# Kernel optimization log

Hardware: AMD Instinct MI355X
Metric: run time of the kernel (lower is better)

Reference implementation:

```python
import jax, jax.numpy as jnp
import numpy as np

FEATURE_SIZE = 128
NUM_BINS = 5
HIDDEN = 512
CONTEXT = 64
N = 65536
PI = float(np.pi)
TAIL_BOUND = 5.0
MIN_BW = 1e-3
MIN_BH = 1e-3
MIN_D = 1e-3

_circ = np.array([1] * 64 + [0] * 64)
_trans = np.array(([0] * 32 + [1] * 32) * 2)
_fi = np.arange(FEATURE_SIZE)
IDX_IC = jnp.array(_fi[(_trans <= 0) & (_circ > 0)])   # identity circular (32)
IDX_IR = jnp.array(_fi[(_trans <= 0) & (_circ <= 0)])  # identity regular (32)
IDX_TC = jnp.array(_fi[(_trans > 0) & (_circ > 0)])    # transform circular (32)
IDX_TR = jnp.array(_fi[(_trans > 0) & (_circ <= 0)])   # transform regular (32)
NET_IN = 2 * IDX_IC.shape[0] + IDX_IR.shape[0]                                  # 96
NET_OUT = IDX_TC.shape[0] * NUM_BINS * 3 + IDX_TR.shape[0] * (NUM_BINS * 3 + 1) # 992


def _rq_spline(x, uw, uh, ud, left, right, bottom, top):
    """Monotonic rational-quadratic spline (nflows-style), forward direction.
    x: [N, D]; uw, uh: [N, D, K]; ud: [N, D, K+1]. Returns (y, logabsdet)."""
    K = uw.shape[-1]
    widths = jax.nn.softmax(uw, axis=-1)
    widths = MIN_BW + (1.0 - MIN_BW * K) * widths
    cumw = jnp.concatenate([jnp.zeros(widths.shape[:-1] + (1,), widths.dtype),
                            jnp.cumsum(widths, axis=-1)], axis=-1)
    cumw = left + (right - left) * cumw
    cumw = cumw.at[..., -1].set(right)
    widths = cumw[..., 1:] - cumw[..., :-1]

    heights = jax.nn.softmax(uh, axis=-1)
    heights = MIN_BH + (1.0 - MIN_BH * K) * heights
    cumh = jnp.concatenate([jnp.zeros(heights.shape[:-1] + (1,), heights.dtype),
                            jnp.cumsum(heights, axis=-1)], axis=-1)
    cumh = bottom + (top - bottom) * cumh
    cumh = cumh.at[..., -1].set(top)
    heights = cumh[..., 1:] - cumh[..., :-1]

    derivs = MIN_D + jax.nn.softplus(ud)  # [N, D, K+1]
    delta = heights / widths              # bin slopes

    xc = jnp.clip(x, left, right)
    # per-element bin search over knot positions
    idx = jnp.clip(jnp.sum(xc[..., None] >= cumw[..., 1:], axis=-1), 0, K - 1)

    def g(a, i):
        return jnp.take_along_axis(a, i[..., None], axis=-1)[..., 0]

    in_cw = g(cumw[..., :-1], idx)
    in_w = g(widths, idx)
    in_ch = g(cumh[..., :-1], idx)
    in_h = g(heights, idx)
    in_delta = g(delta, idx)
    d_k = g(derivs, idx)
    d_k1 = g(derivs, idx + 1)

    theta = (xc - in_cw) / in_w
    omt = 1.0 - theta
    num = in_h * (in_delta * theta * theta + d_k * theta * omt)
    den = in_delta + (d_k + d_k1 - 2.0 * in_delta) * theta * omt
    y = in_ch + num / den
    dnum = in_delta * in_delta * (d_k1 * theta * theta
                                  + 2.0 * in_delta * theta * omt
                                  + d_k * omt * omt)
    logabsdet = jnp.log(dnum) - 2.0 * jnp.log(den)
    return y, logabsdet


def setup_inputs() -> dict:
    key = jax.random.key(0)
    ks = jax.random.split(key, 6)
    inputs = jax.random.uniform(ks[0], (N, FEATURE_SIZE), jnp.float32)
    context = jax.random.normal(ks[1], (N, CONTEXT), jnp.float32)
    fan1 = NET_IN + CONTEXT
    W1 = jax.random.normal(ks[2], (fan1, HIDDEN), jnp.float32) / np.sqrt(fan1)
    b1 = jnp.zeros((HIDDEN,), jnp.float32)
    W2 = jax.random.normal(ks[3], (HIDDEN, HIDDEN), jnp.float32) / np.sqrt(HIDDEN)
    b2 = jnp.zeros((HIDDEN,), jnp.float32)
    W3 = jax.random.normal(ks[4], (HIDDEN, NET_OUT), jnp.float32) / np.sqrt(HIDDEN)
    b3 = jnp.zeros((NET_OUT,), jnp.float32)
    return {"inputs": inputs, "context": context,
            "W1": W1, "b1": b1, "W2": W2, "b2": b2, "W3": W3, "b3": b3}


def reference(inputs, context, W1, b1, W2, b2, W3, b3):
    ic = inputs[..., IDX_IC]
    ir = inputs[..., IDX_IR]
    tc = inputs[..., IDX_TC]
    tr = inputs[..., IDX_TR]

    # conditioner MLP on [cos(ic), sin(ic), ir, context]
    net_in = jnp.concatenate([jnp.cos(ic), jnp.sin(ic), ir, context], axis=-1)
    h = jax.nn.relu(net_in @ W1 + b1)
    h = jax.nn.relu(h @ W2 + b2)
    params = h @ W3 + b3  # [N, 992]

    ntc = IDX_TC.shape[0]
    ntr = IDX_TR.shape[0]
    K = NUM_BINS
    scale = 1.0 / np.sqrt(HIDDEN)

    cc = params[..., : ntc * 3 * K].reshape(-1, ntc, 3 * K)
    cr = params[..., ntc * 3 * K:].reshape(-1, ntr, 3 * K + 1)

    # circular spline on [-pi, pi] with periodic derivative (K derivs, wrap first)
    uw_c = cc[..., :K] * scale
    uh_c = cc[..., K:2 * K] * scale
    ud_c = cc[..., 2 * K:]
    ud_c = jnp.concatenate([ud_c, ud_c[..., :1]], axis=-1)
    yc, lad_c = _rq_spline(tc, uw_c, uh_c, ud_c, -PI, PI, -PI, PI)

    # regular spline on [-B, B] with K+1 derivatives; identity (linear tails) outside
    uw_r = cr[..., :K] * scale
    uh_r = cr[..., K:2 * K] * scale
    ud_r = cr[..., 2 * K:]
    inside = (tr >= -TAIL_BOUND) & (tr <= TAIL_BOUND)
    yr0, lad_r0 = _rq_spline(tr, uw_r, uh_r, ud_r,
                             -TAIL_BOUND, TAIL_BOUND, -TAIL_BOUND, TAIL_BOUND)
    yr = jnp.where(inside, yr0, tr)
    lad_r = jnp.where(inside, lad_r0, 0.0)

    outputs = jnp.zeros_like(inputs)
    outputs = outputs.at[..., IDX_IC].set(ic)
    outputs = outputs.at[..., IDX_IR].set(ir)
    outputs = outputs.at[..., IDX_TC].set(yc)
    outputs = outputs.at[..., IDX_TR].set(yr)
    logabsdet = jnp.sum(lad_c, axis=-1) + jnp.sum(lad_r, axis=-1)
    return outputs, logabsdet
```

## Files before the change

### kernel.cpp

```cpp
#include <hip/hip_runtime.h>
#include <hip/hip_bf16.h>
#include <cstdint>
#include <cstddef>


#define BM 128
#define BN 128
#define BK 64

typedef float  f32x4 __attribute__((ext_vector_type(4)));
typedef short  s16x8 __attribute__((ext_vector_type(8)));

__device__ __forceinline__ void mfma_bf16_16x16x32(f32x4& acc, s16x8 a, s16x8 b) {
    asm volatile("v_mfma_f32_16x16x32_bf16 %0, %1, %2, %0"
                 : "+v"(acc) : "v"(a), "v"(b));
}

__device__ __forceinline__ void gload_lds16(const void* g, void* lds) {
    __builtin_amdgcn_global_load_lds((const __attribute__((address_space(1))) void*)g,
                                     (__attribute__((address_space(3))) void*)lds,
                                     16, 0, 0);
}

__device__ __forceinline__ float bf2f(short s) {
    union { unsigned u; float f; } v;
    v.u = ((unsigned)(unsigned short)s) << 16;
    return v.f;
}


__global__ void prep_input_kernel(const float* __restrict__ inputs,
                                  const float* __restrict__ context,
                                  __hip_bfloat16* __restrict__ netin)
{
    const int n = blockIdx.x;
    const int c = threadIdx.x;
    float v;
    if (c < 32)       v = cosf(inputs[(size_t)n * 128 + c]);
    else if (c < 64)  v = sinf(inputs[(size_t)n * 128 + (c - 32)]);
    else if (c < 96)  v = inputs[(size_t)n * 128 + c];
    else if (c < 160) v = context[(size_t)n * 64 + (c - 96)];
    else              v = 0.f;
    netin[(size_t)n * 192 + c] = __float2bfloat16(v);
}

__global__ void prep_weights_kernel(const float* __restrict__ W1,
                                    const float* __restrict__ W2,
                                    const float* __restrict__ W3,
                                    const float* __restrict__ b3,
                                    __hip_bfloat16* __restrict__ W1T,
                                    __hip_bfloat16* __restrict__ W2T,
                                    __hip_bfloat16* __restrict__ W3T,
                                    float* __restrict__ b3p)
{
    const int T1 = 512 * 192, T2 = 512 * 512, T3 = 1024 * 512;
    const int total = T1 + T2 + T3 + 1024;
    for (int t = blockIdx.x * blockDim.x + threadIdx.x; t < total;
         t += gridDim.x * blockDim.x) {
        if (t < T1) {
            int nn = t / 192, k = t % 192;
            float v = (k < 160) ? W1[(size_t)k * 512 + nn] : 0.f;
            W1T[t] = __float2bfloat16(v);
        } else if (t < T1 + T2) {
            int u = t - T1;
            int nn = u / 512, k = u % 512;
            W2T[u] = __float2bfloat16(W2[(size_t)k * 512 + nn]);
        } else if (t < T1 + T2 + T3) {
            int u = t - T1 - T2;
            int nn = u / 512, k = u % 512;
            float v = (nn < 992) ? W3[(size_t)k * 992 + nn] : 0.f;
            W3T[u] = __float2bfloat16(v);
        } else {
            int u = t - T1 - T2 - T3;
            b3p[u] = (u < 992) ? b3[u] : 0.f;
        }
    }
}


template<bool RELU>
__global__ __launch_bounds__(256)
void gemm_bt_kernel(const __hip_bfloat16* __restrict__ A,
                    const __hip_bfloat16* __restrict__ BT,
                    const float* __restrict__ bias,
                    __hip_bfloat16* __restrict__ C,
                    int M, int Nc, int K)
{
    __shared__ __align__(16) short Ald[BM * BK];
    __shared__ __align__(16) short Bld[BN * BK];

    const int tid  = threadIdx.x;
    const int wid  = tid >> 6;
    const int lane = tid & 63;
    const int row0 = blockIdx.y * BM;
    const int col0 = blockIdx.x * BN;
    const int wr   = (wid >> 1) * 64;
    const int wc   = (wid & 1) * 64;

    f32x4 acc[4][4] = {};

    const int srow  = lane >> 3;
    const int scolb = (lane & 7) * 16;

    const char* Abase = (const char*)A  + (size_t)row0 * K * 2;
    const char* Bbase = (const char*)BT + (size_t)col0 * K * 2;

    const int fr = lane & 15;
    const int fq = lane >> 4;

    const int nk = K / BK;
    for (int kt = 0; kt < nk; ++kt) {
        __syncthreads();
#pragma unroll
        for (int i = 0; i < 4; ++i) {
            const int chunk = i * 4 + wid;
            const int r = chunk * 8 + srow;
            gload_lds16(Abase + ((size_t)r * K + (size_t)kt * BK) * 2 + scolb,
                        (char*)Ald + chunk * 1024);
            gload_lds16(Bbase + ((size_t)r * K + (size_t)kt * BK) * 2 + scolb,
                        (char*)Bld + chunk * 1024);
        }
        __syncthreads();
#pragma unroll
        for (int kk = 0; kk < 2; ++kk) {
            s16x8 af[4], bfv[4];
#pragma unroll
            for (int m = 0; m < 4; ++m)
                af[m] = *(const s16x8*)&Ald[(wr + m * 16 + fr) * BK + kk * 32 + fq * 8];
#pragma unroll
            for (int n = 0; n < 4; ++n)
                bfv[n] = *(const s16x8*)&Bld[(wc + n * 16 + fr) * BK + kk * 32 + fq * 8];
#pragma unroll
            for (int m = 0; m < 4; ++m)
#pragma unroll
                for (int n = 0; n < 4; ++n)
                    mfma_bf16_16x16x32(acc[m][n], af[m], bfv[n]);
        }
    }

#pragma unroll
    for (int n = 0; n < 4; ++n) {
        const int col = col0 + wc + n * 16 + fr;
        const float bv = bias[col];
#pragma unroll
        for (int m = 0; m < 4; ++m) {
            const int rbase = row0 + wr + m * 16 + fq * 4;
#pragma unroll
            for (int r = 0; r < 4; ++r) {
                float v = acc[m][n][r] + bv;
                if (RELU) v = fmaxf(v, 0.f);
                C[(size_t)(rbase + r) * Nc + col] = __float2bfloat16(v);
            }
        }
    }
}


__global__ __launch_bounds__(256)
void spline_kernel(const float* __restrict__ inputs,
                   const __hip_bfloat16* __restrict__ params,
                   float* __restrict__ out, int Nrows)
{
    __shared__ __align__(16) short plds[4][1024];
    const int wid  = threadIdx.x >> 6;
    const int lane = threadIdx.x & 63;
    const int row  = blockIdx.x * 4 + wid;

    const short* prow = (const short*)params + (size_t)row * 1024;
    for (int c = lane; c < 124; c += 64)
        ((int4*)&plds[wid][0])[c] = ((const int4*)prow)[c];
    __syncthreads();

    const bool circ = lane < 32;
    const int  j    = circ ? lane : lane - 32;
    const float PI_F  = 3.14159265358979323846f;
    const float left  = circ ? -PI_F : -5.0f;
    const float right = -left;
    const float SCALE = 0.04419417382415922f;

    const short* pp = &plds[wid][circ ? j * 15 : 480 + j * 16];

    float uw[5], uh[5], ud[6];
#pragma unroll
    for (int i = 0; i < 5; ++i) uw[i] = bf2f(pp[i]) * SCALE;
#pragma unroll
    for (int i = 0; i < 5; ++i) uh[i] = bf2f(pp[5 + i]) * SCALE;
    if (circ) {
#pragma unroll
        for (int i = 0; i < 5; ++i) ud[i] = bf2f(pp[10 + i]);
        ud[5] = ud[0];
    } else {
#pragma unroll
        for (int i = 0; i < 6; ++i) ud[i] = bf2f(pp[10 + i]);
    }

    const int xcol = circ ? (32 + j) : (96 + j);
    const float x  = inputs[(size_t)row * 128 + xcol];

    float mx = uw[0];
#pragma unroll
    for (int i = 1; i < 5; ++i) mx = fmaxf(mx, uw[i]);
    float e[5], s = 0.f;
#pragma unroll
    for (int i = 0; i < 5; ++i) { e[i] = __expf(uw[i] - mx); s += e[i]; }
    const float inv_s = 1.f / s;
    float cw[6];
    cw[0] = left;
    {
        float accw = 0.f;
#pragma unroll
        for (int i = 0; i < 5; ++i) {
            float wn = 0.001f + 0.995f * (e[i] * inv_s);
            accw += wn;
            cw[i + 1] = left + (right - left) * accw;
        }
    }
    cw[5] = right;

    float mh = uh[0];
#pragma unroll
    for (int i = 1; i < 5; ++i) mh = fmaxf(mh, uh[i]);
    float eh[5], sh = 0.f;
#pragma unroll
    for (int i = 0; i < 5; ++i) { eh[i] = __expf(uh[i] - mh); sh += eh[i]; }
    const float inv_sh = 1.f / sh;
    float ch[6];
    ch[0] = left;
    {
        float acch = 0.f;
#pragma unroll
        for (int i = 0; i < 5; ++i) {
            float hn = 0.001f + 0.995f * (eh[i] * inv_sh);
            acch += hn;
            ch[i + 1] = left + (right - left) * acch;
        }
    }
    ch[5] = right;

    float d[6];
#pragma unroll
    for (int i = 0; i < 6; ++i) {
        float u  = ud[i];
        float sp = fmaxf(u, 0.f) + log1pf(__expf(-fabsf(u)));
        d[i] = 0.001f + sp;
    }

    const float xc = fminf(fmaxf(x, left), right);
    int b = 0;
#pragma unroll
    for (int i = 1; i <= 5; ++i) b += (xc >= cw[i]) ? 1 : 0;
    b = (b > 4) ? 4 : b;

    float l_cw = cw[0], r_cw = cw[1], l_ch = ch[0], r_ch = ch[1], dk = d[0], dk1 = d[1];
#pragma unroll
    for (int i = 1; i < 5; ++i) {
        if (b == i) {
            l_cw = cw[i]; r_cw = cw[i + 1];
            l_ch = ch[i]; r_ch = ch[i + 1];
            dk   = d[i];  dk1  = d[i + 1];
        }
    }

    const float iw  = r_cw - l_cw;
    const float ih  = r_ch - l_ch;
    const float del = ih / iw;
    const float th  = (xc - l_cw) / iw;
    const float omt = 1.f - th;
    const float num = ih * (del * th * th + dk * th * omt);
    const float den = del + (dk + dk1 - 2.f * del) * th * omt;
    float y = l_ch + num / den;
    const float dnum = del * del * (dk1 * th * th + 2.f * del * th * omt + dk * omt * omt);
    float lad = __logf(dnum) - 2.f * __logf(den);

    if (!circ) {
        const bool inside = (x >= -5.0f) && (x <= 5.0f);
        if (!inside) { y = x; lad = 0.f; }
    }

    const int ccol = circ ? j : 64 + j;
    out[(size_t)row * 128 + ccol] = inputs[(size_t)row * 128 + ccol];
    out[(size_t)row * 128 + xcol] = y;

    float t = lad;
#pragma unroll
    for (int o = 32; o > 0; o >>= 1) t += __shfl_xor(t, o, 64);
    if (lane == 0) out[(size_t)Nrows * 128 + row] = t;
}


extern "C" void kernel_launch(void* const* d_in, const int* in_sizes, int n_in,
                              void* d_out, int out_size, void* d_ws, size_t ws_size,
                              hipStream_t stream)
{
    const float* inputs  = (const float*)d_in[0];
    const float* context = (const float*)d_in[1];
    const float* W1 = (const float*)d_in[2];
    const float* b1 = (const float*)d_in[3];
    const float* W2 = (const float*)d_in[4];
    const float* b2 = (const float*)d_in[5];
    const float* W3 = (const float*)d_in[6];
    const float* b3 = (const float*)d_in[7];
    float* out = (float*)d_out;

    const int Nrows = in_sizes[0] / 128;

    char* ws = (char*)d_ws;
    const size_t szh    = (size_t)Nrows * 512 * 2;
    const size_t sznet  = (size_t)Nrows * 192 * 2;
    const size_t szpar  = (size_t)Nrows * 1024 * 2;
    const size_t off_h2     = 0;
    const size_t off_netin  = szh;
    const size_t off_h1     = szh + sznet;
    const size_t off_params = szh;
    const size_t off_w1t    = szh + szpar;
    const size_t off_w2t    = off_w1t + (size_t)512 * 192 * 2;
    const size_t off_w3t    = off_w2t + (size_t)512 * 512 * 2;
    const size_t off_b3p    = off_w3t + (size_t)1024 * 512 * 2;

    __hip_bfloat16* netin  = (__hip_bfloat16*)(ws + off_netin);
    __hip_bfloat16* h1     = (__hip_bfloat16*)(ws + off_h1);
    __hip_bfloat16* h2     = (__hip_bfloat16*)(ws + off_h2);
    __hip_bfloat16* params = (__hip_bfloat16*)(ws + off_params);
    __hip_bfloat16* W1T    = (__hip_bfloat16*)(ws + off_w1t);
    __hip_bfloat16* W2T    = (__hip_bfloat16*)(ws + off_w2t);
    __hip_bfloat16* W3T    = (__hip_bfloat16*)(ws + off_w3t);
    float*          b3p    = (float*)(ws + off_b3p);

    prep_weights_kernel<<<2048, 256, 0, stream>>>(W1, W2, W3, b3, W1T, W2T, W3T, b3p);
    prep_input_kernel<<<Nrows, 192, 0, stream>>>(inputs, context, netin);

    gemm_bt_kernel<true ><<<dim3(4, Nrows / 128), 256, 0, stream>>>(
        netin, W1T, b1, h1, Nrows, 512, 192);
    gemm_bt_kernel<true ><<<dim3(4, Nrows / 128), 256, 0, stream>>>(
        h1, W2T, b2, h2, Nrows, 512, 512);
    gemm_bt_kernel<false><<<dim3(8, Nrows / 128), 256, 0, stream>>>(
        h2, W3T, b3p, params, Nrows, 1024, 512);

    spline_kernel<<<Nrows / 4, 256, 0, stream>>>(inputs, params, out, Nrows);
}
```

Before: 305.7 us.

## Fuse input prep, three-layer MLP and spline into one per-tile kernel

Replaces the separate prep, three GEMM and spline kernels with one kernel that processes 64 rows per block. Activations stay in swizzled LDS across layers and the final layer is split into two halves so each spline half reads parameters from LDS. W3 and the bias are repacked so each feature's parameters sit at a 16-element stride. This removes the global round trips for the hidden activations and parameters. In exchange it uses about 152KB of LDS per block, which allows only one block per CU with 8 waves, and the weights are read directly from global/L2 by every block without LDS staging.

```diff
diff --git a/kernel.cpp b/kernel.cpp
--- a/kernel.cpp
+++ b/kernel.cpp
@@ -4,45 +4,20 @@
 #include <cstddef>
 
 
-#define BM 128
-#define BN 128
-#define BK 64
-
 typedef float  f32x4 __attribute__((ext_vector_type(4)));
 typedef short  s16x8 __attribute__((ext_vector_type(8)));
 
-__device__ __forceinline__ void mfma_bf16_16x16x32(f32x4& acc, s16x8 a, s16x8 b) {
-    asm volatile("v_mfma_f32_16x16x32_bf16 %0, %1, %2, %0"
-                 : "+v"(acc) : "v"(a), "v"(b));
-}
-
-__device__ __forceinline__ void gload_lds16(const void* g, void* lds) {
-    __builtin_amdgcn_global_load_lds((const __attribute__((address_space(1))) void*)g,
-                                     (__attribute__((address_space(3))) void*)lds,
-                                     16, 0, 0);
-}
-
+__device__ __forceinline__ void mfma16(f32x4& acc, s16x8 a, s16x8 b) {
+    asm volatile("v_mfma_f32_16x16x32_bf16 %0, %1, %2, %0" : "+v"(acc) : "v"(a), "v"(b));
+}
 __device__ __forceinline__ float bf2f(short s) {
-    union { unsigned u; float f; } v;
-    v.u = ((unsigned)(unsigned short)s) << 16;
-    return v.f;
-}
-
-
-__global__ void prep_input_kernel(const float* __restrict__ inputs,
-                                  const float* __restrict__ context,
-                                  __hip_bfloat16* __restrict__ netin)
-{
-    const int n = blockIdx.x;
-    const int c = threadIdx.x;
-    float v;
-    if (c < 32)       v = cosf(inputs[(size_t)n * 128 + c]);
-    else if (c < 64)  v = sinf(inputs[(size_t)n * 128 + (c - 32)]);
-    else if (c < 96)  v = inputs[(size_t)n * 128 + c];
-    else if (c < 160) v = context[(size_t)n * 64 + (c - 96)];
-    else              v = 0.f;
-    netin[(size_t)n * 192 + c] = __float2bfloat16(v);
-}
+    union { unsigned u; float f; } v; v.u = ((unsigned)(unsigned short)s) << 16; return v.f;
+}
+__device__ __forceinline__ short f2bf(float f) {
+    __hip_bfloat16 h = __float2bfloat16(f); return *(short*)&h;
+}
+__device__ __forceinline__ int swz(int row) { return ((row ^ (row >> 3)) & 7) << 4; }
+
 
 __global__ void prep_weights_kernel(const float* __restrict__ W1,
                                     const float* __restrict__ W2,
@@ -67,135 +42,102 @@
             W2T[u] = __float2bfloat16(W2[(size_t)k * 512 + nn]);
         } else if (t < T1 + T2 + T3) {
             int u = t - T1 - T2;
-            int nn = u / 512, k = u % 512;
-            float v = (nn < 992) ? W3[(size_t)k * 992 + nn] : 0.f;
+            int c = u / 512, k = u % 512;
+            int f = c >> 4, p = c & 15;
+            float v = 0.f;
+            if (f < 32) { if (p < 15) v = W3[(size_t)k * 992 + f * 15 + p]; }
+            else        {              v = W3[(size_t)k * 992 + 480 + (f - 32) * 16 + p]; }
             W3T[u] = __float2bfloat16(v);
         } else {
-            int u = t - T1 - T2 - T3;
-            b3p[u] = (u < 992) ? b3[u] : 0.f;
-        }
-    }
-}
-
-
-template<bool RELU>
-__global__ __launch_bounds__(256)
-void gemm_bt_kernel(const __hip_bfloat16* __restrict__ A,
-                    const __hip_bfloat16* __restrict__ BT,
-                    const float* __restrict__ bias,
-                    __hip_bfloat16* __restrict__ C,
-                    int M, int Nc, int K)
-{
-    __shared__ __align__(16) short Ald[BM * BK];
-    __shared__ __align__(16) short Bld[BN * BK];
-
-    const int tid  = threadIdx.x;
-    const int wid  = tid >> 6;
-    const int lane = tid & 63;
-    const int row0 = blockIdx.y * BM;
-    const int col0 = blockIdx.x * BN;
-    const int wr   = (wid >> 1) * 64;
-    const int wc   = (wid & 1) * 64;
-
+            int c = t - T1 - T2 - T3;
+            int f = c >> 4, p = c & 15;
+            float v = 0.f;
+            if (f < 32) { if (p < 15) v = b3[f * 15 + p]; }
+            else        {              v = b3[480 + (f - 32) * 16 + p]; }
+            b3p[c] = v;
+        }
+    }
+}
+
+
+template<int K, bool RELU>
+__device__ __forceinline__ void layer_gemm(
+    const char* Alds, int lda,
+    const short* __restrict__ Bg,
+    const float* __restrict__ bias, int bias0,
+    int col0,
+    char* Hdst, int ldh,
+    int lane)
+{
+    const int fr = lane & 15, fq = lane >> 4;
     f32x4 acc[4][4] = {};
-
-    const int srow  = lane >> 3;
-    const int scolb = (lane & 7) * 16;
-
-    const char* Abase = (const char*)A  + (size_t)row0 * K * 2;
-    const char* Bbase = (const char*)BT + (size_t)col0 * K * 2;
-
-    const int fr = lane & 15;
-    const int fq = lane >> 4;
-
-    const int nk = K / BK;
-    for (int kt = 0; kt < nk; ++kt) {
-        __syncthreads();
-#pragma unroll
-        for (int i = 0; i < 4; ++i) {
-            const int chunk = i * 4 + wid;
-            const int r = chunk * 8 + srow;
-            gload_lds16(Abase + ((size_t)r * K + (size_t)kt * BK) * 2 + scolb,
-                        (char*)Ald + chunk * 1024);
-            gload_lds16(Bbase + ((size_t)r * K + (size_t)kt * BK) * 2 + scolb,
-                        (char*)Bld + chunk * 1024);
-        }
-        __syncthreads();
-#pragma unroll
-        for (int kk = 0; kk < 2; ++kk) {
-            s16x8 af[4], bfv[4];
-#pragma unroll
-            for (int m = 0; m < 4; ++m)
-                af[m] = *(const s16x8*)&Ald[(wr + m * 16 + fr) * BK + kk * 32 + fq * 8];
+    const short* brow[4];
+#pragma unroll
+    for (int n = 0; n < 4; ++n)
+        brow[n] = Bg + (size_t)(col0 + n * 16 + fr) * K;
+    const char* arow[4]; int asw[4];
+#pragma unroll
+    for (int m = 0; m < 4; ++m) {
+        const int r = m * 16 + fr;
+        arow[m] = Alds + r * lda;
+        asw[m]  = swz(r);
+    }
+#pragma unroll 4
+    for (int kk = 0; kk < K / 32; ++kk) {
+        s16x8 a[4], b[4];
+#pragma unroll
+        for (int n = 0; n < 4; ++n)
+            b[n] = *(const s16x8*)(brow[n] + kk * 32 + fq * 8);
+#pragma unroll
+        for (int m = 0; m < 4; ++m)
+            a[m] = *(const s16x8*)(arow[m] + ((kk * 64 + fq * 16) ^ asw[m]));
+#pragma unroll
+        for (int m = 0; m < 4; ++m)
 #pragma unroll
             for (int n = 0; n < 4; ++n)
-                bfv[n] = *(const s16x8*)&Bld[(wc + n * 16 + fr) * BK + kk * 32 + fq * 8];
-#pragma unroll
-            for (int m = 0; m < 4; ++m)
-#pragma unroll
-                for (int n = 0; n < 4; ++n)
-                    mfma_bf16_16x16x32(acc[m][n], af[m], bfv[n]);
-        }
-    }
-
+                mfma16(acc[m][n], a[m], b[n]);
+    }
 #pragma unroll
     for (int n = 0; n < 4; ++n) {
-        const int col = col0 + wc + n * 16 + fr;
-        const float bv = bias[col];
+        const int col = col0 + n * 16 + fr;
+        const float bv = bias[bias0 + col];
 #pragma unroll
         for (int m = 0; m < 4; ++m) {
-            const int rbase = row0 + wr + m * 16 + fq * 4;
 #pragma unroll
             for (int r = 0; r < 4; ++r) {
+                const int row = m * 16 + fq * 4 + r;
                 float v = acc[m][n][r] + bv;
                 if (RELU) v = fmaxf(v, 0.f);
-                C[(size_t)(rbase + r) * Nc + col] = __float2bfloat16(v);
+                *(short*)(Hdst + row * ldh + ((col * 2) ^ swz(row))) = f2bf(v);
             }
         }
     }
 }
 
 
-__global__ __launch_bounds__(256)
-void spline_kernel(const float* __restrict__ inputs,
-                   const __hip_bfloat16* __restrict__ params,
-                   float* __restrict__ out, int Nrows)
-{
-    __shared__ __align__(16) short plds[4][1024];
-    const int wid  = threadIdx.x >> 6;
-    const int lane = threadIdx.x & 63;
-    const int row  = blockIdx.x * 4 + wid;
-
-    const short* prow = (const short*)params + (size_t)row * 1024;
-    for (int c = lane; c < 124; c += 64)
-        ((int4*)&plds[wid][0])[c] = ((const int4*)prow)[c];
-    __syncthreads();
-
-    const bool circ = lane < 32;
-    const int  j    = circ ? lane : lane - 32;
+template<int CH>
+__device__ __forceinline__ float spline_eval(s16x8 p0, s16x8 p1,
+                                             const float* __restrict__ inputs,
+                                             float* __restrict__ out,
+                                             size_t grow, int f)
+{
     const float PI_F  = 3.14159265358979323846f;
-    const float left  = circ ? -PI_F : -5.0f;
+    const float left  = (CH == 0) ? -PI_F : -5.0f;
     const float right = -left;
     const float SCALE = 0.04419417382415922f;
 
-    const short* pp = &plds[wid][circ ? j * 15 : 480 + j * 16];
-
     float uw[5], uh[5], ud[6];
-#pragma unroll
-    for (int i = 0; i < 5; ++i) uw[i] = bf2f(pp[i]) * SCALE;
-#pragma unroll
-    for (int i = 0; i < 5; ++i) uh[i] = bf2f(pp[5 + i]) * SCALE;
-    if (circ) {
-#pragma unroll
-        for (int i = 0; i < 5; ++i) ud[i] = bf2f(pp[10 + i]);
-        ud[5] = ud[0];
-    } else {
-#pragma unroll
-        for (int i = 0; i < 6; ++i) ud[i] = bf2f(pp[10 + i]);
-    }
-
-    const int xcol = circ ? (32 + j) : (96 + j);
-    const float x  = inputs[(size_t)row * 128 + xcol];
+    uw[0] = bf2f(p0[0]) * SCALE; uw[1] = bf2f(p0[1]) * SCALE; uw[2] = bf2f(p0[2]) * SCALE;
+    uw[3] = bf2f(p0[3]) * SCALE; uw[4] = bf2f(p0[4]) * SCALE;
+    uh[0] = bf2f(p0[5]) * SCALE; uh[1] = bf2f(p0[6]) * SCALE; uh[2] = bf2f(p0[7]) * SCALE;
+    uh[3] = bf2f(p1[0]) * SCALE; uh[4] = bf2f(p1[1]) * SCALE;
+    ud[0] = bf2f(p1[2]); ud[1] = bf2f(p1[3]); ud[2] = bf2f(p1[4]);
+    ud[3] = bf2f(p1[5]); ud[4] = bf2f(p1[6]);
+    ud[5] = (CH == 0) ? ud[0] : bf2f(p1[7]);
+
+    const int xcol = (CH == 0) ? 32 + f : 96 + f;
+    const int ccol = (CH == 0) ? f : 64 + f;
+    const float x = inputs[grow * 128 + xcol];
 
     float mx = uw[0];
 #pragma unroll
@@ -207,12 +149,11 @@
     float cw[6];
     cw[0] = left;
     {
-        float accw = 0.f;
+        float a = 0.f;
 #pragma unroll
         for (int i = 0; i < 5; ++i) {
-            float wn = 0.001f + 0.995f * (e[i] * inv_s);
-            accw += wn;
-            cw[i + 1] = left + (right - left) * accw;
+            a += 0.001f + 0.995f * (e[i] * inv_s);
+            cw[i + 1] = left + (right - left) * a;
         }
     }
     cw[5] = right;
@@ -227,12 +168,11 @@
     float ch[6];
     ch[0] = left;
     {
-        float acch = 0.f;
+        float a = 0.f;
 #pragma unroll
         for (int i = 0; i < 5; ++i) {
-            float hn = 0.001f + 0.995f * (eh[i] * inv_sh);
-            acch += hn;
-            ch[i + 1] = left + (right - left) * acch;
+            a += 0.001f + 0.995f * (eh[i] * inv_sh);
+            ch[i + 1] = left + (right - left) * a;
         }
     }
     ch[5] = right;
@@ -241,8 +181,7 @@
 #pragma unroll
     for (int i = 0; i < 6; ++i) {
         float u  = ud[i];
-        float sp = fmaxf(u, 0.f) + log1pf(__expf(-fabsf(u)));
-        d[i] = 0.001f + sp;
+        d[i] = 0.001f + fmaxf(u, 0.f) + log1pf(__expf(-fabsf(u)));
     }
 
     const float xc = fminf(fmaxf(x, left), right);
@@ -272,19 +211,90 @@
     const float dnum = del * del * (dk1 * th * th + 2.f * del * th * omt + dk * omt * omt);
     float lad = __logf(dnum) - 2.f * __logf(den);
 
-    if (!circ) {
+    if (CH == 1) {
         const bool inside = (x >= -5.0f) && (x <= 5.0f);
         if (!inside) { y = x; lad = 0.f; }
     }
 
-    const int ccol = circ ? j : 64 + j;
-    out[(size_t)row * 128 + ccol] = inputs[(size_t)row * 128 + ccol];
-    out[(size_t)row * 128 + xcol] = y;
-
-    float t = lad;
-#pragma unroll
-    for (int o = 32; o > 0; o >>= 1) t += __shfl_xor(t, o, 64);
-    if (lane == 0) out[(size_t)Nrows * 128 + row] = t;
+    out[grow * 128 + ccol] = inputs[grow * 128 + ccol];
+    out[grow * 128 + xcol] = y;
+    return lad;
+}
+
+
+__global__ __launch_bounds__(512)
+void fused_mlp_spline(const float* __restrict__ inputs, const float* __restrict__ context,
+                      const short* __restrict__ W1T, const float* __restrict__ b1,
+                      const short* __restrict__ W2T, const float* __restrict__ b2,
+                      const short* __restrict__ W3T, const float* __restrict__ b3p,
+                      float* __restrict__ out, int Nrows)
+{
+    __shared__ __align__(16) char smem[155648];
+    char* A1  = smem;
+    char* H1  = smem + 24576;
+    char* H2  = smem + 90112;
+    char* PAR = smem;
+
+    const int tid  = threadIdx.x;
+    const int w    = tid >> 6;
+    const int lane = tid & 63;
+    const int row0 = blockIdx.x * 64;
+
+    {
+        const int r  = tid >> 3;
+        const int cb = (tid & 7) * 24;
+        const float* inr = inputs  + (size_t)(row0 + r) * 128;
+        const float* ctr = context + (size_t)(row0 + r) * 64;
+        const int sw = swz(r);
+#pragma unroll
+        for (int j = 0; j < 24; ++j) {
+            const int c = cb + j;
+            float v;
+            if      (c < 32)  v = cosf(inr[c]);
+            else if (c < 64)  v = sinf(inr[c - 32]);
+            else if (c < 96)  v = inr[c];
+            else if (c < 160) v = ctr[c - 96];
+            else              v = 0.f;
+            *(short*)(A1 + r * 384 + ((c * 2) ^ sw)) = f2bf(v);
+        }
+    }
+    __syncthreads();
+    layer_gemm<192, true >(A1, 384,  W1T, b1, 0,   w * 64, H1, 1024, lane);
+    __syncthreads();
+    layer_gemm<512, true >(H1, 1024, W2T, b2, 0,   w * 64, H2, 1024, lane);
+    __syncthreads();
+
+    float lad_acc[4];
+
+    layer_gemm<512, false>(H2, 1024, W3T, b3p, 0,  w * 64, PAR, 1024, lane);
+    __syncthreads();
+#pragma unroll
+    for (int it = 0; it < 4; ++it) {
+        const int row = w * 8 + it * 2 + (lane >> 5);
+        const int f   = lane & 31;
+        const char* base = PAR + row * 1024;
+        const int sw = swz(row);
+        s16x8 p0 = *(const s16x8*)(base + ((f * 32)      ^ sw));
+        s16x8 p1 = *(const s16x8*)(base + ((f * 32 + 16) ^ sw));
+        lad_acc[it] = spline_eval<0>(p0, p1, inputs, out, (size_t)row0 + row, f);
+    }
+    __syncthreads();
+
+    layer_gemm<512, false>(H2, 1024, W3T + (size_t)512 * 512, b3p, 512, w * 64, PAR, 1024, lane);
+    __syncthreads();
+#pragma unroll
+    for (int it = 0; it < 4; ++it) {
+        const int row = w * 8 + it * 2 + (lane >> 5);
+        const int f   = lane & 31;
+        const char* base = PAR + row * 1024;
+        const int sw = swz(row);
+        s16x8 p0 = *(const s16x8*)(base + ((f * 32)      ^ sw));
+        s16x8 p1 = *(const s16x8*)(base + ((f * 32 + 16) ^ sw));
+        float lad = lad_acc[it] + spline_eval<1>(p0, p1, inputs, out, (size_t)row0 + row, f);
+#pragma unroll
+        for (int o = 16; o > 0; o >>= 1) lad += __shfl_xor(lad, o, 64);
+        if ((lane & 31) == 0) out[(size_t)Nrows * 128 + row0 + row] = lad;
+    }
 }
 
 
@@ -305,36 +315,15 @@
     const int Nrows = in_sizes[0] / 128;
 
     char* ws = (char*)d_ws;
-    const size_t szh    = (size_t)Nrows * 512 * 2;
-    const size_t sznet  = (size_t)Nrows * 192 * 2;
-    const size_t szpar  = (size_t)Nrows * 1024 * 2;
-    const size_t off_h2     = 0;
-    const size_t off_netin  = szh;
-    const size_t off_h1     = szh + sznet;
-    const size_t off_params = szh;
-    const size_t off_w1t    = szh + szpar;
-    const size_t off_w2t    = off_w1t + (size_t)512 * 192 * 2;
-    const size_t off_w3t    = off_w2t + (size_t)512 * 512 * 2;
-    const size_t off_b3p    = off_w3t + (size_t)1024 * 512 * 2;
-
-    __hip_bfloat16* netin  = (__hip_bfloat16*)(ws + off_netin);
-    __hip_bfloat16* h1     = (__hip_bfloat16*)(ws + off_h1);
-    __hip_bfloat16* h2     = (__hip_bfloat16*)(ws + off_h2);
-    __hip_bfloat16* params = (__hip_bfloat16*)(ws + off_params);
-    __hip_bfloat16* W1T    = (__hip_bfloat16*)(ws + off_w1t);
-    __hip_bfloat16* W2T    = (__hip_bfloat16*)(ws + off_w2t);
-    __hip_bfloat16* W3T    = (__hip_bfloat16*)(ws + off_w3t);
-    float*          b3p    = (float*)(ws + off_b3p);
+    __hip_bfloat16* W1T = (__hip_bfloat16*)(ws);
+    __hip_bfloat16* W2T = (__hip_bfloat16*)(ws + 196608);
+    __hip_bfloat16* W3T = (__hip_bfloat16*)(ws + 720896);
+    float*          b3p = (float*)         (ws + 1769472);
 
     prep_weights_kernel<<<2048, 256, 0, stream>>>(W1, W2, W3, b3, W1T, W2T, W3T, b3p);
-    prep_input_kernel<<<Nrows, 192, 0, stream>>>(inputs, context, netin);
-
-    gemm_bt_kernel<true ><<<dim3(4, Nrows / 128), 256, 0, stream>>>(
-        netin, W1T, b1, h1, Nrows, 512, 192);
-    gemm_bt_kernel<true ><<<dim3(4, Nrows / 128), 256, 0, stream>>>(
-        h1, W2T, b2, h2, Nrows, 512, 512);
-    gemm_bt_kernel<false><<<dim3(8, Nrows / 128), 256, 0, stream>>>(
-        h2, W3T, b3p, params, Nrows, 1024, 512);
-
-    spline_kernel<<<Nrows / 4, 256, 0, stream>>>(inputs, params, out, Nrows);
-}
+
+    fused_mlp_spline<<<Nrows / 64, 512, 0, stream>>>(
+        inputs, context,
+        (const short*)W1T, b1, (const short*)W2T, b2, (const short*)W3T, b3p,
+        out, Nrows);
+}
```

After: 391.5 us. +28.1%, slower.
